# Kernel optimization log

Hardware: AMD Instinct MI355X
Metric: run time of the kernel (lower is better)

## Reference

```python
import jax, jax.numpy as jnp
import numpy as np

N_NODES = 50000
N_EDGES = 800000
IN_CH, HID, OUT_CH = 3, 64, 768
NEG_SLOPE = 0.01  # torch LeakyReLU default
BN_EPS = 1e-5


def _gcn_conv(x, edge_index, W, b):
    # PyG GCNConv: add self-loops, symmetric degree normalization, scatter-add.
    n = x.shape[0]
    loops = jnp.arange(n, dtype=edge_index.dtype)
    src = jnp.concatenate([edge_index[0], loops])
    dst = jnp.concatenate([edge_index[1], loops])
    deg = jax.ops.segment_sum(jnp.ones(src.shape[0], x.dtype), dst, num_segments=n)
    dinv = jnp.where(deg > 0, jax.lax.rsqrt(deg), 0.0)
    norm = dinv[src] * dinv[dst]                      # [E+N]
    h = x @ W                                          # [N, out]
    msg = h[src] * norm[:, None]                       # gather + edge scale
    return jax.ops.segment_sum(msg, dst, num_segments=n) + b


def _block(x, edge_index, W, b, gamma, beta):
    h = _gcn_conv(x, edge_index, W, b)
    h = jnp.where(h >= 0, h, NEG_SLOPE * h)            # LeakyReLU
    mean = h.mean(axis=0)
    var = h.var(axis=0)                                # biased, as torch BN train
    h = (h - mean) * jax.lax.rsqrt(var + BN_EPS) * gamma + beta
    return h                                           # dropout: identity (eval)


def _glorot(key, fan_in, fan_out):
    s = np.sqrt(6.0 / (fan_in + fan_out)).astype(np.float32)
    return jax.random.uniform(key, (fan_in, fan_out), jnp.float32, -s, s)


def setup_inputs() -> dict:
    key = jax.random.key(0)
    ks = jax.random.split(key, 8)
    x = jax.random.normal(ks[0], (N_NODES, IN_CH), jnp.float32)
    edge_index = jax.random.randint(ks[1], (2, N_EDGES), 0, N_NODES, jnp.int64)
    inp = {"x": x, "edge_index": edge_index}
    inp["W1"] = _glorot(ks[2], IN_CH, HID)
    inp["b1"] = jnp.zeros((HID,), jnp.float32)
    inp["g1"] = jnp.ones((HID,), jnp.float32)
    inp["be1"] = jnp.zeros((HID,), jnp.float32)
    inp["W2"] = _glorot(ks[3], HID, HID)
    inp["b2"] = jnp.zeros((HID,), jnp.float32)
    inp["g2"] = jnp.ones((HID,), jnp.float32)
    inp["be2"] = jnp.zeros((HID,), jnp.float32)
    inp["W3"] = _glorot(ks[4], HID, HID)
    inp["b3"] = jnp.zeros((HID,), jnp.float32)
    inp["g3"] = jnp.ones((HID,), jnp.float32)
    inp["be3"] = jnp.zeros((HID,), jnp.float32)
    inp["Wmu"] = _glorot(ks[5], HID, OUT_CH)
    inp["bmu"] = jnp.zeros((OUT_CH,), jnp.float32)
    inp["Wls"] = _glorot(ks[6], HID, OUT_CH)
    inp["bls"] = jnp.zeros((OUT_CH,), jnp.float32)
    return inp


def reference(x, edge_index, W1, b1, g1, be1, W2, b2, g2, be2, W3, b3, g3, be3, Wmu, bmu, Wls, bls):
    h = _block(x, edge_index, W1, b1, g1, be1)
    h = _block(h, edge_index, W2, b2, g2, be2)
    h = _block(h, edge_index, W3, b3, g3, be3)
    mu = _gcn_conv(h, edge_index, Wmu, bmu)
    logstd = _gcn_conv(h, edge_index, Wls, bls)
    return (mu, logstd)
```

## Files before the change

### kernel.cpp

```cpp
#include <hip/hip_runtime.h>
#include <cstddef>


#define NEG_SLOPE 0.01f
#define BN_EPS 1e-5f

__global__ __launch_bounds__(256) void init_k(int* __restrict__ cnt,
                                              float* __restrict__ bns, int N) {
  int i = blockIdx.x * 256 + threadIdx.x;
  if (i < N) cnt[i] = 0;
  if (i < 384) bns[i] = 0.0f;
}

__global__ __launch_bounds__(256) void hist_k(const int* __restrict__ dst,
                                              int* __restrict__ cnt, int E) {
  int e = blockIdx.x * 256 + threadIdx.x;
  if (e < E) atomicAdd(&cnt[dst[e]], 1);
}

__global__ __launch_bounds__(1024) void scanA(const int* __restrict__ cnt,
                                              int* __restrict__ pre,
                                              int* __restrict__ bsum, int N) {
  __shared__ int sh[1024];
  const int t = threadIdx.x;
  const int i = blockIdx.x * 1024 + t;
  int c = (i < N) ? cnt[i] : 0;
  sh[t] = c;
  __syncthreads();
  for (int off = 1; off < 1024; off <<= 1) {
    int v = (t >= off) ? sh[t - off] : 0;
    __syncthreads();
    sh[t] += v;
    __syncthreads();
  }
  if (i < N) pre[i] = sh[t] - c;
  if (t == 1023) bsum[blockIdx.x] = sh[t];
}

__global__ __launch_bounds__(64) void scanB(int* __restrict__ bsum, int nb) {
  int t = threadIdx.x;
  int orig = (t < nb) ? bsum[t] : 0;
  int v = orig;
#pragma unroll
  for (int off = 1; off < 64; off <<= 1) {
    int u = __shfl_up(v, off);
    if (t >= off) v += u;
  }
  if (t < nb) bsum[t] = v - orig;
}

__global__ __launch_bounds__(256) void scanC(const int* __restrict__ cnt,
                                             int* __restrict__ rowptr,
                                             int* __restrict__ cursor,
                                             const int* __restrict__ bsum,
                                             float* __restrict__ dinv,
                                             int N, int E) {
  int i = blockIdx.x * 256 + threadIdx.x;
  if (i < N) {
    int rp = rowptr[i] + bsum[i >> 10];
    rowptr[i] = rp;
    cursor[i] = rp;
    dinv[i] = rsqrtf((float)(cnt[i] + 1));
  }
  if (i == 0) rowptr[N] = E;
}

__global__ __launch_bounds__(256) void fill_k(const int* __restrict__ src,
                                              const int* __restrict__ dst,
                                              int* __restrict__ cursor,
                                              int* __restrict__ eidx, int E) {
  int e = blockIdx.x * 256 + threadIdx.x;
  if (e >= E) return;
  int p = atomicAdd(&cursor[dst[e]], 1);
  eidx[p] = src[e];
}

__global__ __launch_bounds__(256) void l1_fused(
    const int* __restrict__ rowptr, const int* __restrict__ eidx,
    const float* __restrict__ x, const float* __restrict__ dinv,
    const float* __restrict__ W1, const float* __restrict__ b1,
    float* __restrict__ Z, float* __restrict__ q, float* __restrict__ bns, int N) {
  const int t = threadIdx.x, lane = t & 63, wid = t >> 6;
  const int gw = blockIdx.x * 4 + wid;
  const int nw = gridDim.x * 4;
  const float w0 = W1[lane], w1 = W1[64 + lane], w2 = W1[128 + lane];
  const float bb = b1[lane];
  float s1 = 0.f, s2 = 0.f;
  for (int node = gw; node < N; node += nw) {
    int beg = rowptr[node], end = rowptr[node + 1];
    float a0 = 0.f, a1 = 0.f, a2 = 0.f, aq = 0.f;
    for (int e = beg + lane; e < end; e += 64) {
      int s = eidx[e];
      float dv = dinv[s];
      a0 += x[s * 3] * dv;
      a1 += x[s * 3 + 1] * dv;
      a2 += x[s * 3 + 2] * dv;
      aq += dv;
    }
#pragma unroll
    for (int off = 32; off; off >>= 1) {
      a0 += __shfl_xor(a0, off);
      a1 += __shfl_xor(a1, off);
      a2 += __shfl_xor(a2, off);
      aq += __shfl_xor(aq, off);
    }
    float dv = dinv[node];
    a0 += x[node * 3] * dv;
    a1 += x[node * 3 + 1] * dv;
    a2 += x[node * 3 + 2] * dv;
    aq += dv;
    float u = dv * (a0 * w0 + a1 * w1 + a2 * w2) + bb;
    float o = u >= 0.f ? u : NEG_SLOPE * u;
    Z[(size_t)node * 64 + lane] = o * dv;
    s1 += o;
    s2 += o * o;
    if (lane == 0) q[node] = aq;
  }
  __shared__ float red[8][64];
  red[wid][lane] = s1;
  red[4 + wid][lane] = s2;
  __syncthreads();
  if (t < 64) {
    atomicAdd(&bns[t], red[0][t] + red[1][t] + red[2][t] + red[3][t]);
    atomicAdd(&bns[64 + t], red[4][t] + red[5][t] + red[6][t] + red[7][t]);
  }
}

__global__ __launch_bounds__(256) void gather64(const int* __restrict__ rowptr,
                                                const int* __restrict__ eidx,
                                                const float* __restrict__ Z,
                                                float* __restrict__ G, int N) {
  int node = blockIdx.x * 4 + (threadIdx.x >> 6);
  if (node >= N) return;
  int lane = threadIdx.x & 63;
  int slot = lane >> 4;
  int c4 = (lane & 15) << 2;
  int beg = rowptr[node], end = rowptr[node + 1];
  float ax = 0.f, ay = 0.f, az = 0.f, aw = 0.f;
  int e = beg + slot;
  for (; e + 4 < end; e += 8) {
    int s0 = eidx[e], s1 = eidx[e + 4];
    float4 v0 = *(const float4*)(Z + (size_t)s0 * 64 + c4);
    float4 v1 = *(const float4*)(Z + (size_t)s1 * 64 + c4);
    ax += v0.x + v1.x;
    ay += v0.y + v1.y;
    az += v0.z + v1.z;
    aw += v0.w + v1.w;
  }
  if (e < end) {
    int s0 = eidx[e];
    float4 v0 = *(const float4*)(Z + (size_t)s0 * 64 + c4);
    ax += v0.x; ay += v0.y; az += v0.z; aw += v0.w;
  }
#pragma unroll
  for (int off = 16; off < 64; off <<= 1) {
    ax += __shfl_xor(ax, off);
    ay += __shfl_xor(ay, off);
    az += __shfl_xor(az, off);
    aw += __shfl_xor(aw, off);
  }
  if (slot == 0) {
    float4 self = *(const float4*)(Z + (size_t)node * 64 + c4);
    float4 o = make_float4(ax + self.x, ay + self.y, az + self.z, aw + self.w);
    *(float4*)(G + (size_t)node * 64 + c4) = o;
  }
}

__global__ __launch_bounds__(256) void prep_small(
    const float* __restrict__ bns, const float* __restrict__ g,
    const float* __restrict__ be, const float* __restrict__ W,
    float* __restrict__ Wc, float* __restrict__ cx, float invN) {
  __shared__ float sc[64], sh[64], part[4][64];
  int t = threadIdx.x;
  if (t < 64) {
    float mean = bns[t] * invN;
    float var = bns[64 + t] * invN - mean * mean;
    float s = g[t] * rsqrtf(var + BN_EPS);
    sc[t] = s;
    sh[t] = be[t] - mean * s;
  }
  __syncthreads();
  int c = t & 63, kq = t >> 6;
  float p = 0.f;
  for (int k = kq * 16; k < kq * 16 + 16; ++k) {
    float w = W[k * 64 + c];
    Wc[k * 64 + c] = sc[k] * w;
    p += sh[k] * w;
  }
  part[kq][c] = p;
  __syncthreads();
  if (t < 64) cx[t] = part[0][t] + part[1][t] + part[2][t] + part[3][t];
}

__global__ __launch_bounds__(256) void prep_head(
    const float* __restrict__ bns, const float* __restrict__ g,
    const float* __restrict__ be, const float* __restrict__ Wmu,
    const float* __restrict__ Wls, float* __restrict__ Wmc,
    float* __restrict__ Wlc, float* __restrict__ cmu, float* __restrict__ cls,
    float invN) {
  __shared__ float sc[64], sh[64], part[2][128];
  int t = threadIdx.x;
  if (t < 64) {
    float mean = bns[t] * invN;
    float var = bns[64 + t] * invN - mean * mean;
    float s = g[t] * rsqrtf(var + BN_EPS);
    sc[t] = s;
    sh[t] = be[t] - mean * s;
  }
  __syncthreads();
  int blk = blockIdx.x;
  int head = blk >= 6 ? 1 : 0;
  int c0 = (head ? blk - 6 : blk) * 128;
  const float* W = head ? Wls : Wmu;
  float* Wc = head ? Wlc : Wmc;
  float* cx = head ? cls : cmu;
  int c = c0 + (t & 127), kh = t >> 7;
  float p = 0.f;
  for (int k = kh * 32; k < kh * 32 + 32; ++k) {
    float w = W[(size_t)k * 768 + c];
    Wc[(size_t)k * 768 + c] = sc[k] * w;
    p += sh[k] * w;
  }
  part[kh][t & 127] = p;
  __syncthreads();
  if (t < 128) cx[c0 + t] = part[0][t] + part[1][t];
}

__global__ __launch_bounds__(256, 4) void gemm_bnq(
    const float* __restrict__ G, const float* __restrict__ dinv,
    const float* __restrict__ q, const float* __restrict__ Wc,
    const float* __restrict__ cx, const float* __restrict__ b,
    float* __restrict__ Z, float* __restrict__ bns, int N) {
  __shared__ __align__(16) float P[64][68];
  __shared__ __align__(16) float Ws[64][64];
  const int t = threadIdx.x;
  const int r0 = blockIdx.x * 64;

  for (int i = t; i < 1024; i += 256) {
    int r = i >> 4, k4 = (i & 15) << 2, gr = r0 + r;
    float4 v = make_float4(0.f, 0.f, 0.f, 0.f);
    if (gr < N) v = *(const float4*)(G + (size_t)gr * 64 + k4);
    *(float4*)&P[r][k4] = v;
  }
  for (int i = t; i < 4096; i += 256) Ws[i >> 6][i & 63] = Wc[i];
  __syncthreads();

  const int tr = t >> 4, tc4 = (t & 15) << 2;
  float acc[4][4] = {};
#pragma unroll 8
  for (int k = 0; k < 64; ++k) {
    float4 w = *(const float4*)&Ws[k][tc4];
#pragma unroll
    for (int i = 0; i < 4; ++i) {
      float a = P[tr + 16 * i][k];
      acc[i][0] += a * w.x;
      acc[i][1] += a * w.y;
      acc[i][2] += a * w.z;
      acc[i][3] += a * w.w;
    }
  }

  float s1[4] = {0.f, 0.f, 0.f, 0.f}, s2[4] = {0.f, 0.f, 0.f, 0.f};
  float4 bb = *(const float4*)(b + tc4);
  float4 cc = *(const float4*)(cx + tc4);
#pragma unroll
  for (int i = 0; i < 4; ++i) {
    int r = r0 + tr + 16 * i;
    if (r < N) {
      float dv = dinv[r];
      float dq = dv * q[r];
      float u0 = acc[i][0] * dv + dq * cc.x + bb.x;
      float u1 = acc[i][1] * dv + dq * cc.y + bb.y;
      float u2 = acc[i][2] * dv + dq * cc.z + bb.z;
      float u3 = acc[i][3] * dv + dq * cc.w + bb.w;
      float o0 = u0 >= 0.f ? u0 : NEG_SLOPE * u0;
      float o1 = u1 >= 0.f ? u1 : NEG_SLOPE * u1;
      float o2 = u2 >= 0.f ? u2 : NEG_SLOPE * u2;
      float o3 = u3 >= 0.f ? u3 : NEG_SLOPE * u3;
      float4 z = make_float4(o0 * dv, o1 * dv, o2 * dv, o3 * dv);
      *(float4*)(Z + (size_t)r * 64 + tc4) = z;
      s1[0] += o0; s2[0] += o0 * o0;
      s1[1] += o1; s2[1] += o1 * o1;
      s1[2] += o2; s2[2] += o2 * o2;
      s1[3] += o3; s2[3] += o3 * o3;
    }
  }
  __syncthreads();
  float (*red1)[64] = (float(*)[64]) & Ws[0][0];
  float (*red2)[64] = (float(*)[64]) & Ws[16][0];
#pragma unroll
  for (int j = 0; j < 4; ++j) {
    red1[tr][tc4 + j] = s1[j];
    red2[tr][tc4 + j] = s2[j];
  }
  __syncthreads();
  if (t < 64) {
    float a1 = 0.f, a2 = 0.f;
#pragma unroll
    for (int i = 0; i < 16; ++i) {
      a1 += red1[i][t];
      a2 += red2[i][t];
    }
    atomicAdd(&bns[t], a1);
    atomicAdd(&bns[64 + t], a2);
  }
}

__global__ __launch_bounds__(256, 4) void head_gemm2(
    const float* __restrict__ G, const float* __restrict__ dinv,
    const float* __restrict__ q, const float* __restrict__ Wmc,
    const float* __restrict__ cmu, const float* __restrict__ bmu,
    const float* __restrict__ Wlc, const float* __restrict__ cls,
    const float* __restrict__ bls, float* __restrict__ OUT, int N) {
  __shared__ __align__(16) float P[64][68];
  __shared__ __align__(16) float Ws[32][128];
  const int t = threadIdx.x;
  const int r0 = blockIdx.x * 64;
  const int yy = blockIdx.y;
  const int head = (yy >= 6) ? 1 : 0;
  const int c0 = (head ? yy - 6 : yy) * 128;
  const float* W = head ? Wlc : Wmc;
  const float* cx = head ? cls : cmu;
  const float* b = head ? bls : bmu;
  float* O = OUT + (head ? (size_t)N * 768 : 0);

  for (int i = t; i < 1024; i += 256) {
    int r = i >> 4, k4 = (i & 15) << 2, gr = r0 + r;
    float4 v = make_float4(0.f, 0.f, 0.f, 0.f);
    if (gr < N) v = *(const float4*)(G + (size_t)gr * 64 + k4);
    *(float4*)&P[r][k4] = v;
  }

  const int tr = t >> 4;
  const int tc = t & 15;
  float acc[4][8] = {};

  for (int kk = 0; kk < 64; kk += 32) {
    __syncthreads();
    for (int i = t; i < 1024; i += 256) {
      int k = i >> 5, c4 = (i & 31) << 2;
      *(float4*)&Ws[k][c4] = *(const float4*)(W + (size_t)(kk + k) * 768 + c0 + c4);
    }
    __syncthreads();
#pragma unroll 4
    for (int k = 0; k < 32; ++k) {
      float4 w0 = *(const float4*)&Ws[k][tc * 4];
      float4 w1 = *(const float4*)&Ws[k][64 + tc * 4];
      float a[4];
      a[0] = P[tr][kk + k];
      a[1] = P[tr + 16][kk + k];
      a[2] = P[tr + 32][kk + k];
      a[3] = P[tr + 48][kk + k];
#pragma unroll
      for (int i = 0; i < 4; ++i) {
        acc[i][0] += a[i] * w0.x;
        acc[i][1] += a[i] * w0.y;
        acc[i][2] += a[i] * w0.z;
        acc[i][3] += a[i] * w0.w;
        acc[i][4] += a[i] * w1.x;
        acc[i][5] += a[i] * w1.y;
        acc[i][6] += a[i] * w1.z;
        acc[i][7] += a[i] * w1.w;
      }
    }
  }

  float4 bb0 = *(const float4*)(b + c0 + tc * 4);
  float4 bb1 = *(const float4*)(b + c0 + 64 + tc * 4);
  float4 cc0 = *(const float4*)(cx + c0 + tc * 4);
  float4 cc1 = *(const float4*)(cx + c0 + 64 + tc * 4);
#pragma unroll
  for (int i = 0; i < 4; ++i) {
    int r = r0 + tr + 16 * i;
    if (r < N) {
      float dv = dinv[r];
      float dq = dv * q[r];
      float4 o0 = make_float4(acc[i][0] * dv + dq * cc0.x + bb0.x,
                              acc[i][1] * dv + dq * cc0.y + bb0.y,
                              acc[i][2] * dv + dq * cc0.z + bb0.z,
                              acc[i][3] * dv + dq * cc0.w + bb0.w);
      float4 o1 = make_float4(acc[i][4] * dv + dq * cc1.x + bb1.x,
                              acc[i][5] * dv + dq * cc1.y + bb1.y,
                              acc[i][6] * dv + dq * cc1.z + bb1.z,
                              acc[i][7] * dv + dq * cc1.w + bb1.w);
      *(float4*)(O + (size_t)r * 768 + c0 + tc * 4) = o0;
      *(float4*)(O + (size_t)r * 768 + c0 + 64 + tc * 4) = o1;
    }
  }
}

extern "C" void kernel_launch(void* const* d_in, const int* in_sizes, int n_in,
                              void* d_out, int out_size, void* d_ws, size_t ws_size,
                              hipStream_t stream) {
  const float* x   = (const float*)d_in[0];
  const int*   ei  = (const int*)d_in[1];
  const float* W1  = (const float*)d_in[2];
  const float* b1  = (const float*)d_in[3];
  const float* g1  = (const float*)d_in[4];
  const float* be1 = (const float*)d_in[5];
  const float* W2  = (const float*)d_in[6];
  const float* b2  = (const float*)d_in[7];
  const float* g2  = (const float*)d_in[8];
  const float* be2 = (const float*)d_in[9];
  const float* W3  = (const float*)d_in[10];
  const float* b3  = (const float*)d_in[11];
  const float* g3  = (const float*)d_in[12];
  const float* be3 = (const float*)d_in[13];
  const float* Wmu = (const float*)d_in[14];
  const float* bmu = (const float*)d_in[15];
  const float* Wls = (const float*)d_in[16];
  const float* bls = (const float*)d_in[17];

  const int N = in_sizes[0] / 3;
  const int E = in_sizes[1] / 2;
  const int* src = ei;
  const int* dst = ei + E;
  float* out = (float*)d_out;

  char* ws = (char*)d_ws;
  size_t o = 0;
  float* dinv = (float*)(ws + o); o += (size_t)N * 4;
  float* qv   = (float*)(ws + o); o += (size_t)N * 4;
  float* bns  = (float*)(ws + o); o += 384 * 4;
  float* W2c  = (float*)(ws + o); o += 4096 * 4;
  float* c2   = (float*)(ws + o); o += 64 * 4;
  float* W3c  = (float*)(ws + o); o += 4096 * 4;
  float* c3   = (float*)(ws + o); o += 64 * 4;
  float* Wmc  = (float*)(ws + o); o += (size_t)64 * 768 * 4;
  float* cmu  = (float*)(ws + o); o += 768 * 4;
  float* Wlc  = (float*)(ws + o); o += (size_t)64 * 768 * 4;
  float* cls  = (float*)(ws + o); o += 768 * 4;
  int* cnt    = (int*)(ws + o);   o += (size_t)N * 4;
  int* rowptr = (int*)(ws + o);   o += ((size_t)N + 1) * 4;
  int* cursor = (int*)(ws + o);   o += (size_t)N * 4;
  int* bsum   = (int*)(ws + o);   o += 64 * 4;
  int* eidx   = (int*)(ws + o);   o += (size_t)E * 4;
  float* B0   = (float*)(ws + o); o += (size_t)N * 64 * 4;
  float* B1   = (float*)(ws + o); o += (size_t)N * 64 * 4;

  const float invN = 1.0f / (float)N;
  int nbN = (N + 255) / 256;
  int nbE = (E + 255) / 256;
  int gb  = (N + 63) / 64;
  int wb  = (N + 3) / 4;
  int sbA = (N + 1023) / 1024;

  init_k<<<nbN, 256, 0, stream>>>(cnt, bns, N);
  hist_k<<<nbE, 256, 0, stream>>>(dst, cnt, E);
  scanA<<<sbA, 1024, 0, stream>>>(cnt, rowptr, bsum, N);
  scanB<<<1, 64, 0, stream>>>(bsum, sbA);
  scanC<<<nbN, 256, 0, stream>>>(cnt, rowptr, cursor, bsum, dinv, N, E);
  fill_k<<<nbE, 256, 0, stream>>>(src, dst, cursor, eidx, E);

  l1_fused<<<1024, 256, 0, stream>>>(rowptr, eidx, x, dinv, W1, b1, B0, qv, bns, N);
  prep_small<<<1, 256, 0, stream>>>(bns + 0, g1, be1, W2, W2c, c2, invN);

  gather64<<<wb, 256, 0, stream>>>(rowptr, eidx, B0, B1, N);
  gemm_bnq<<<gb, 256, 0, stream>>>(B1, dinv, qv, W2c, c2, b2, B0, bns + 128, N);
  prep_small<<<1, 256, 0, stream>>>(bns + 128, g2, be2, W3, W3c, c3, invN);

  gather64<<<wb, 256, 0, stream>>>(rowptr, eidx, B0, B1, N);
  gemm_bnq<<<gb, 256, 0, stream>>>(B1, dinv, qv, W3c, c3, b3, B0, bns + 256, N);
  prep_head<<<12, 256, 0, stream>>>(bns + 256, g3, be3, Wmu, Wls, Wmc, Wlc, cmu, cls, invN);

  gather64<<<wb, 256, 0, stream>>>(rowptr, eidx, B0, B1, N);
  dim3 hgrid(gb, 12);
  head_gemm2<<<hgrid, 256, 0, stream>>>(B1, dinv, qv, Wmc, cmu, bmu, Wlc, cls, bls, out, N);
}
```

Before: 444.7 us.

## Fuse neighbor gather into GEMM kernels and loop head chunks per block

The CSR neighbor aggregation is moved into the GEMM kernels, which now build each 64-row tile directly in shared memory instead of launching a separate gather that writes and rereads an intermediate buffer. The head kernel now gathers once per row tile and loops over all 12 output column chunks for both heads, rather than using a 2D grid that reloaded the tile per chunk. This removes intermediate global traffic and three launches, but reduces grid parallelism for the head kernel and serializes 16 rows of gather per wave, which may hurt latency hiding.

```diff
diff --git a/kernel.cpp b/kernel.cpp
--- a/kernel.cpp
+++ b/kernel.cpp
@@ -126,43 +126,50 @@
   }
 }
 
-__global__ __launch_bounds__(256) void gather64(const int* __restrict__ rowptr,
-                                                const int* __restrict__ eidx,
-                                                const float* __restrict__ Z,
-                                                float* __restrict__ G, int N) {
-  int node = blockIdx.x * 4 + (threadIdx.x >> 6);
-  if (node >= N) return;
-  int lane = threadIdx.x & 63;
-  int slot = lane >> 4;
-  int c4 = (lane & 15) << 2;
-  int beg = rowptr[node], end = rowptr[node + 1];
-  float ax = 0.f, ay = 0.f, az = 0.f, aw = 0.f;
-  int e = beg + slot;
-  for (; e + 4 < end; e += 8) {
-    int s0 = eidx[e], s1 = eidx[e + 4];
-    float4 v0 = *(const float4*)(Z + (size_t)s0 * 64 + c4);
-    float4 v1 = *(const float4*)(Z + (size_t)s1 * 64 + c4);
-    ax += v0.x + v1.x;
-    ay += v0.y + v1.y;
-    az += v0.z + v1.z;
-    aw += v0.w + v1.w;
-  }
-  if (e < end) {
-    int s0 = eidx[e];
-    float4 v0 = *(const float4*)(Z + (size_t)s0 * 64 + c4);
-    ax += v0.x; ay += v0.y; az += v0.z; aw += v0.w;
-  }
-#pragma unroll
-  for (int off = 16; off < 64; off <<= 1) {
-    ax += __shfl_xor(ax, off);
-    ay += __shfl_xor(ay, off);
-    az += __shfl_xor(az, off);
-    aw += __shfl_xor(aw, off);
-  }
-  if (slot == 0) {
-    float4 self = *(const float4*)(Z + (size_t)node * 64 + c4);
-    float4 o = make_float4(ax + self.x, ay + self.y, az + self.z, aw + self.w);
-    *(float4*)(G + (size_t)node * 64 + c4) = o;
+__device__ __forceinline__ void gather_tile(
+    const int* __restrict__ rowptr, const int* __restrict__ eidx,
+    const float* __restrict__ Z, float (*__restrict__ P)[68], int r0, int N) {
+  const int t = threadIdx.x;
+  const int lane = t & 63, wid = t >> 6;
+  const int slot = lane >> 4, c4 = (lane & 15) << 2;
+#pragma unroll 1
+  for (int i = 0; i < 16; ++i) {
+    const int r = wid * 16 + i;
+    const int gr = r0 + r;
+    float ax = 0.f, ay = 0.f, az = 0.f, aw = 0.f;
+    if (gr < N) {
+      const int beg = rowptr[gr], end = rowptr[gr + 1];
+      int e = beg + slot;
+      for (; e + 4 < end; e += 8) {
+        int s0 = eidx[e], s1 = eidx[e + 4];
+        float4 v0 = *(const float4*)(Z + (size_t)s0 * 64 + c4);
+        float4 v1 = *(const float4*)(Z + (size_t)s1 * 64 + c4);
+        ax += v0.x + v1.x;
+        ay += v0.y + v1.y;
+        az += v0.z + v1.z;
+        aw += v0.w + v1.w;
+      }
+      if (e < end) {
+        int s0 = eidx[e];
+        float4 v0 = *(const float4*)(Z + (size_t)s0 * 64 + c4);
+        ax += v0.x; ay += v0.y; az += v0.z; aw += v0.w;
+      }
+    }
+#pragma unroll
+    for (int off = 16; off < 64; off <<= 1) {
+      ax += __shfl_xor(ax, off);
+      ay += __shfl_xor(ay, off);
+      az += __shfl_xor(az, off);
+      aw += __shfl_xor(aw, off);
+    }
+    if (slot == 0) {
+      float4 o = make_float4(0.f, 0.f, 0.f, 0.f);
+      if (gr < N) {
+        float4 self = *(const float4*)(Z + (size_t)gr * 64 + c4);
+        o = make_float4(ax + self.x, ay + self.y, az + self.z, aw + self.w);
+      }
+      *(float4*)&P[r][c4] = o;
+    }
   }
 }
 
@@ -226,8 +233,9 @@
   if (t < 128) cx[c0 + t] = part[0][t] + part[1][t];
 }
 
-__global__ __launch_bounds__(256, 4) void gemm_bnq(
-    const float* __restrict__ G, const float* __restrict__ dinv,
+__global__ __launch_bounds__(256, 4) void gemm_bnq_f(
+    const int* __restrict__ rowptr, const int* __restrict__ eidx,
+    const float* __restrict__ Zin, const float* __restrict__ dinv,
     const float* __restrict__ q, const float* __restrict__ Wc,
     const float* __restrict__ cx, const float* __restrict__ b,
     float* __restrict__ Z, float* __restrict__ bns, int N) {
@@ -236,13 +244,8 @@
   const int t = threadIdx.x;
   const int r0 = blockIdx.x * 64;
 
-  for (int i = t; i < 1024; i += 256) {
-    int r = i >> 4, k4 = (i & 15) << 2, gr = r0 + r;
-    float4 v = make_float4(0.f, 0.f, 0.f, 0.f);
-    if (gr < N) v = *(const float4*)(G + (size_t)gr * 64 + k4);
-    *(float4*)&P[r][k4] = v;
-  }
   for (int i = t; i < 4096; i += 256) Ws[i >> 6][i & 63] = Wc[i];
+  gather_tile(rowptr, eidx, Zin, P, r0, N);
   __syncthreads();
 
   const int tr = t >> 4, tc4 = (t & 15) << 2;
@@ -306,8 +309,9 @@
   }
 }
 
-__global__ __launch_bounds__(256, 4) void head_gemm2(
-    const float* __restrict__ G, const float* __restrict__ dinv,
+__global__ __launch_bounds__(256, 4) void head_f(
+    const int* __restrict__ rowptr, const int* __restrict__ eidx,
+    const float* __restrict__ Zin, const float* __restrict__ dinv,
     const float* __restrict__ q, const float* __restrict__ Wmc,
     const float* __restrict__ cmu, const float* __restrict__ bmu,
     const float* __restrict__ Wlc, const float* __restrict__ cls,
@@ -316,75 +320,82 @@
   __shared__ __align__(16) float Ws[32][128];
   const int t = threadIdx.x;
   const int r0 = blockIdx.x * 64;
-  const int yy = blockIdx.y;
-  const int head = (yy >= 6) ? 1 : 0;
-  const int c0 = (head ? yy - 6 : yy) * 128;
-  const float* W = head ? Wlc : Wmc;
-  const float* cx = head ? cls : cmu;
-  const float* b = head ? bls : bmu;
-  float* O = OUT + (head ? (size_t)N * 768 : 0);
-
-  for (int i = t; i < 1024; i += 256) {
-    int r = i >> 4, k4 = (i & 15) << 2, gr = r0 + r;
-    float4 v = make_float4(0.f, 0.f, 0.f, 0.f);
-    if (gr < N) v = *(const float4*)(G + (size_t)gr * 64 + k4);
-    *(float4*)&P[r][k4] = v;
-  }
-
   const int tr = t >> 4;
   const int tc = t & 15;
-  float acc[4][8] = {};
-
-  for (int kk = 0; kk < 64; kk += 32) {
-    __syncthreads();
-    for (int i = t; i < 1024; i += 256) {
-      int k = i >> 5, c4 = (i & 31) << 2;
-      *(float4*)&Ws[k][c4] = *(const float4*)(W + (size_t)(kk + k) * 768 + c0 + c4);
-    }
-    __syncthreads();
-#pragma unroll 4
-    for (int k = 0; k < 32; ++k) {
-      float4 w0 = *(const float4*)&Ws[k][tc * 4];
-      float4 w1 = *(const float4*)&Ws[k][64 + tc * 4];
-      float a[4];
-      a[0] = P[tr][kk + k];
-      a[1] = P[tr + 16][kk + k];
-      a[2] = P[tr + 32][kk + k];
-      a[3] = P[tr + 48][kk + k];
-#pragma unroll
-      for (int i = 0; i < 4; ++i) {
-        acc[i][0] += a[i] * w0.x;
-        acc[i][1] += a[i] * w0.y;
-        acc[i][2] += a[i] * w0.z;
-        acc[i][3] += a[i] * w0.w;
-        acc[i][4] += a[i] * w1.x;
-        acc[i][5] += a[i] * w1.y;
-        acc[i][6] += a[i] * w1.z;
-        acc[i][7] += a[i] * w1.w;
-      }
-    }
-  }
-
-  float4 bb0 = *(const float4*)(b + c0 + tc * 4);
-  float4 bb1 = *(const float4*)(b + c0 + 64 + tc * 4);
-  float4 cc0 = *(const float4*)(cx + c0 + tc * 4);
-  float4 cc1 = *(const float4*)(cx + c0 + 64 + tc * 4);
+
+  gather_tile(rowptr, eidx, Zin, P, r0, N);
+
+  float dv4[4], dq4[4];
 #pragma unroll
   for (int i = 0; i < 4; ++i) {
     int r = r0 + tr + 16 * i;
     if (r < N) {
-      float dv = dinv[r];
-      float dq = dv * q[r];
-      float4 o0 = make_float4(acc[i][0] * dv + dq * cc0.x + bb0.x,
-                              acc[i][1] * dv + dq * cc0.y + bb0.y,
-                              acc[i][2] * dv + dq * cc0.z + bb0.z,
-                              acc[i][3] * dv + dq * cc0.w + bb0.w);
-      float4 o1 = make_float4(acc[i][4] * dv + dq * cc1.x + bb1.x,
-                              acc[i][5] * dv + dq * cc1.y + bb1.y,
-                              acc[i][6] * dv + dq * cc1.z + bb1.z,
-                              acc[i][7] * dv + dq * cc1.w + bb1.w);
-      *(float4*)(O + (size_t)r * 768 + c0 + tc * 4) = o0;
-      *(float4*)(O + (size_t)r * 768 + c0 + 64 + tc * 4) = o1;
+      dv4[i] = dinv[r];
+      dq4[i] = dv4[i] * q[r];
+    } else {
+      dv4[i] = 0.f;
+      dq4[i] = 0.f;
+    }
+  }
+
+  for (int chunk = 0; chunk < 12; ++chunk) {
+    const int head = (chunk >= 6) ? 1 : 0;
+    const int c0 = (head ? chunk - 6 : chunk) * 128;
+    const float* W = head ? Wlc : Wmc;
+    const float* cx = head ? cls : cmu;
+    const float* b = head ? bls : bmu;
+    float* O = OUT + (head ? (size_t)N * 768 : 0);
+
+    float acc[4][8] = {};
+    for (int kk = 0; kk < 64; kk += 32) {
+      __syncthreads();
+      for (int i = t; i < 1024; i += 256) {
+        int k = i >> 5, c4 = (i & 31) << 2;
+        *(float4*)&Ws[k][c4] = *(const float4*)(W + (size_t)(kk + k) * 768 + c0 + c4);
+      }
+      __syncthreads();
+#pragma unroll 4
+      for (int k = 0; k < 32; ++k) {
+        float4 w0 = *(const float4*)&Ws[k][tc * 4];
+        float4 w1 = *(const float4*)&Ws[k][64 + tc * 4];
+        float a[4];
+        a[0] = P[tr][kk + k];
+        a[1] = P[tr + 16][kk + k];
+        a[2] = P[tr + 32][kk + k];
+        a[3] = P[tr + 48][kk + k];
+#pragma unroll
+        for (int i = 0; i < 4; ++i) {
+          acc[i][0] += a[i] * w0.x;
+          acc[i][1] += a[i] * w0.y;
+          acc[i][2] += a[i] * w0.z;
+          acc[i][3] += a[i] * w0.w;
+          acc[i][4] += a[i] * w1.x;
+          acc[i][5] += a[i] * w1.y;
+          acc[i][6] += a[i] * w1.z;
+          acc[i][7] += a[i] * w1.w;
+        }
+      }
+    }
+
+    float4 bb0 = *(const float4*)(b + c0 + tc * 4);
+    float4 bb1 = *(const float4*)(b + c0 + 64 + tc * 4);
+    float4 cc0 = *(const float4*)(cx + c0 + tc * 4);
+    float4 cc1 = *(const float4*)(cx + c0 + 64 + tc * 4);
+#pragma unroll
+    for (int i = 0; i < 4; ++i) {
+      int r = r0 + tr + 16 * i;
+      if (r < N) {
+        float4 o0 = make_float4(acc[i][0] * dv4[i] + dq4[i] * cc0.x + bb0.x,
+                                acc[i][1] * dv4[i] + dq4[i] * cc0.y + bb0.y,
+                                acc[i][2] * dv4[i] + dq4[i] * cc0.z + bb0.z,
+                                acc[i][3] * dv4[i] + dq4[i] * cc0.w + bb0.w);
+        float4 o1 = make_float4(acc[i][4] * dv4[i] + dq4[i] * cc1.x + bb1.x,
+                                acc[i][5] * dv4[i] + dq4[i] * cc1.y + bb1.y,
+                                acc[i][6] * dv4[i] + dq4[i] * cc1.z + bb1.z,
+                                acc[i][7] * dv4[i] + dq4[i] * cc1.w + bb1.w);
+        *(float4*)(O + (size_t)r * 768 + c0 + tc * 4) = o0;
+        *(float4*)(O + (size_t)r * 768 + c0 + 64 + tc * 4) = o1;
+      }
     }
   }
 }
@@ -442,7 +453,6 @@
   int nbN = (N + 255) / 256;
   int nbE = (E + 255) / 256;
   int gb  = (N + 63) / 64;
-  int wb  = (N + 3) / 4;
   int sbA = (N + 1023) / 1024;
 
   init_k<<<nbN, 256, 0, stream>>>(cnt, bns, N);
@@ -455,15 +465,14 @@
   l1_fused<<<1024, 256, 0, stream>>>(rowptr, eidx, x, dinv, W1, b1, B0, qv, bns, N);
   prep_small<<<1, 256, 0, stream>>>(bns + 0, g1, be1, W2, W2c, c2, invN);
 
-  gather64<<<wb, 256, 0, stream>>>(rowptr, eidx, B0, B1, N);
-  gemm_bnq<<<gb, 256, 0, stream>>>(B1, dinv, qv, W2c, c2, b2, B0, bns + 128, N);
+  gemm_bnq_f<<<gb, 256, 0, stream>>>(rowptr, eidx, B0, dinv, qv, W2c, c2, b2,
+                                     B1, bns + 128, N);
   prep_small<<<1, 256, 0, stream>>>(bns + 128, g2, be2, W3, W3c, c3, invN);
 
-  gather64<<<wb, 256, 0, stream>>>(rowptr, eidx, B0, B1, N);
-  gemm_bnq<<<gb, 256, 0, stream>>>(B1, dinv, qv, W3c, c3, b3, B0, bns + 256, N);
+  gemm_bnq_f<<<gb, 256, 0, stream>>>(rowptr, eidx, B1, dinv, qv, W3c, c3, b3,
+                                     B0, bns + 256, N);
   prep_head<<<12, 256, 0, stream>>>(bns + 256, g3, be3, Wmu, Wls, Wmc, Wlc, cmu, cls, invN);
 
-  gather64<<<wb, 256, 0, stream>>>(rowptr, eidx, B0, B1, N);
-  dim3 hgrid(gb, 12);
-  head_gemm2<<<hgrid, 256, 0, stream>>>(B1, dinv, qv, Wmc, cmu, bmu, Wlc, cls, bls, out, N);
-}
+  head_f<<<gb, 256, 0, stream>>>(rowptr, eidx, B0, dinv, qv, Wmc, cmu, bmu,
+                                 Wlc, cls, bls, out, N);
+}
```

Measured after the change: 490.0 us. 1.1x slower.

## Fuse neighbor gather into the BN-folded GEMM for hidden layers

Applied to the files above, without the earlier changes.

Layers 2 and 3 no longer run a separate gather kernel that writes the aggregated features to a buffer before the GEMM. Each GEMM block now gathers its 64 rows' neighbor sums directly into shared memory, and the layer output buffers are ping-ponged to match. This removes a kernel launch and a full N×64 write and read per layer. In exchange, each block runs a serial gather loop of 16 rows per wave, which may lower latency hiding compared with the separate high-parallelism gather kernel.

```diff
diff --git a/kernel.cpp b/kernel.cpp
--- a/kernel.cpp
+++ b/kernel.cpp
@@ -166,6 +166,53 @@
   }
 }
 
+__device__ __forceinline__ void gather_tile(
+    const int* __restrict__ rowptr, const int* __restrict__ eidx,
+    const float* __restrict__ Z, float (*__restrict__ P)[68], int r0, int N) {
+  const int t = threadIdx.x;
+  const int lane = t & 63, wid = t >> 6;
+  const int slot = lane >> 4, c4 = (lane & 15) << 2;
+#pragma unroll 1
+  for (int i = 0; i < 16; ++i) {
+    const int r = wid * 16 + i;
+    const int gr = r0 + r;
+    float ax = 0.f, ay = 0.f, az = 0.f, aw = 0.f;
+    if (gr < N) {
+      const int beg = rowptr[gr], end = rowptr[gr + 1];
+      int e = beg + slot;
+      for (; e + 4 < end; e += 8) {
+        int s0 = eidx[e], s1 = eidx[e + 4];
+        float4 v0 = *(const float4*)(Z + (size_t)s0 * 64 + c4);
+        float4 v1 = *(const float4*)(Z + (size_t)s1 * 64 + c4);
+        ax += v0.x + v1.x;
+        ay += v0.y + v1.y;
+        az += v0.z + v1.z;
+        aw += v0.w + v1.w;
+      }
+      if (e < end) {
+        int s0 = eidx[e];
+        float4 v0 = *(const float4*)(Z + (size_t)s0 * 64 + c4);
+        ax += v0.x; ay += v0.y; az += v0.z; aw += v0.w;
+      }
+    }
+#pragma unroll
+    for (int off = 16; off < 64; off <<= 1) {
+      ax += __shfl_xor(ax, off);
+      ay += __shfl_xor(ay, off);
+      az += __shfl_xor(az, off);
+      aw += __shfl_xor(aw, off);
+    }
+    if (slot == 0) {
+      float4 o = make_float4(0.f, 0.f, 0.f, 0.f);
+      if (gr < N) {
+        float4 self = *(const float4*)(Z + (size_t)gr * 64 + c4);
+        o = make_float4(ax + self.x, ay + self.y, az + self.z, aw + self.w);
+      }
+      *(float4*)&P[r][c4] = o;
+    }
+  }
+}
+
 __global__ __launch_bounds__(256) void prep_small(
     const float* __restrict__ bns, const float* __restrict__ g,
     const float* __restrict__ be, const float* __restrict__ W,
@@ -226,8 +273,9 @@
   if (t < 128) cx[c0 + t] = part[0][t] + part[1][t];
 }
 
-__global__ __launch_bounds__(256, 4) void gemm_bnq(
-    const float* __restrict__ G, const float* __restrict__ dinv,
+__global__ __launch_bounds__(256, 4) void gemm_bnq_f(
+    const int* __restrict__ rowptr, const int* __restrict__ eidx,
+    const float* __restrict__ Zin, const float* __restrict__ dinv,
     const float* __restrict__ q, const float* __restrict__ Wc,
     const float* __restrict__ cx, const float* __restrict__ b,
     float* __restrict__ Z, float* __restrict__ bns, int N) {
@@ -236,13 +284,8 @@
   const int t = threadIdx.x;
   const int r0 = blockIdx.x * 64;
 
-  for (int i = t; i < 1024; i += 256) {
-    int r = i >> 4, k4 = (i & 15) << 2, gr = r0 + r;
-    float4 v = make_float4(0.f, 0.f, 0.f, 0.f);
-    if (gr < N) v = *(const float4*)(G + (size_t)gr * 64 + k4);
-    *(float4*)&P[r][k4] = v;
-  }
   for (int i = t; i < 4096; i += 256) Ws[i >> 6][i & 63] = Wc[i];
+  gather_tile(rowptr, eidx, Zin, P, r0, N);
   __syncthreads();
 
   const int tr = t >> 4, tc4 = (t & 15) << 2;
@@ -455,12 +498,12 @@
   l1_fused<<<1024, 256, 0, stream>>>(rowptr, eidx, x, dinv, W1, b1, B0, qv, bns, N);
   prep_small<<<1, 256, 0, stream>>>(bns + 0, g1, be1, W2, W2c, c2, invN);
 
-  gather64<<<wb, 256, 0, stream>>>(rowptr, eidx, B0, B1, N);
-  gemm_bnq<<<gb, 256, 0, stream>>>(B1, dinv, qv, W2c, c2, b2, B0, bns + 128, N);
+  gemm_bnq_f<<<gb, 256, 0, stream>>>(rowptr, eidx, B0, dinv, qv, W2c, c2, b2,
+                                     B1, bns + 128, N);
   prep_small<<<1, 256, 0, stream>>>(bns + 128, g2, be2, W3, W3c, c3, invN);
 
-  gather64<<<wb, 256, 0, stream>>>(rowptr, eidx, B0, B1, N);
-  gemm_bnq<<<gb, 256, 0, stream>>>(B1, dinv, qv, W3c, c3, b3, B0, bns + 256, N);
+  gemm_bnq_f<<<gb, 256, 0, stream>>>(rowptr, eidx, B1, dinv, qv, W3c, c3, b3,
+                                     B0, bns + 256, N);
   prep_head<<<12, 256, 0, stream>>>(bns + 256, g3, be3, Wmu, Wls, Wmc, Wlc, cmu, cls, invN);
 
   gather64<<<wb, 256, 0, stream>>>(rowptr, eidx, B0, B1, N);
```

New measurement: 454.6 us. 1.02x slower.
